# Performance work log

Hardware: AMD Instinct MI355X
Metric: run time of the kernel (lower is better)

Reference implementation:

```python
import jax, jax.numpy as jnp
import numpy as np

DIM = 1024
HIDDEN = 4096
NUM_EXPERTS = 8
TOP_K = 2
T = 8192


def setup_inputs() -> dict:
    key = jax.random.key(0)
    ks = jax.random.split(key, 5)
    scale = 0.02
    x = jax.random.normal(ks[0], (T, DIM), dtype=jnp.float32)
    gate_w = jax.random.normal(ks[1], (NUM_EXPERTS, DIM), dtype=jnp.float32) * scale  # Linear weight [out,in]
    w1 = jax.random.normal(ks[2], (NUM_EXPERTS, HIDDEN, DIM), dtype=jnp.float32) * scale
    w2 = jax.random.normal(ks[3], (NUM_EXPERTS, DIM, HIDDEN), dtype=jnp.float32) * scale
    w3 = jax.random.normal(ks[4], (NUM_EXPERTS, HIDDEN, DIM), dtype=jnp.float32) * scale
    return {"x": x, "gate_w": gate_w, "w1": w1, "w2": w2, "w3": w3}


def reference(x, gate_w, w1, w2, w3):
    # Router: softmax over all experts, take top-2, renormalize.
    logits = jnp.einsum('td,ed->te', x, gate_w)            # [T, E]
    probs = jax.nn.softmax(logits, axis=-1)
    topw, topi = jax.lax.top_k(probs, TOP_K)               # [T, 2]
    topw = topw / jnp.sum(topw, axis=-1, keepdims=True)
    out = jnp.zeros_like(x)
    num_experts = w1.shape[0]
    for e in range(num_experts):
        # combine weight for expert e per token (0 if not routed here)
        w_e = jnp.sum(jnp.where(topi == e, topw, 0.0), axis=-1)   # [T]
        h = jax.nn.silu(x @ w1[e].T) * (x @ w3[e].T)              # [T, HIDDEN]
        out = out + w_e[:, None] * (h @ w2[e].T)                  # [T, DIM]
    return out
```

## Files before the change

### kernel.cpp

```cpp
#include <hip/hip_runtime.h>
#include <hip/hip_bf16.h>
#include <cstdint>
#include <cstddef>

#define TK 8192
#define DIM 1024
#define HID 4096
#define NE 8

typedef __attribute__((ext_vector_type(8))) __bf16 bfrag;
typedef __attribute__((ext_vector_type(4))) float ffrag;

static __device__ __forceinline__ ushort f2bf(float f) {
    union { float f; uint32_t u; } v; v.f = f;
    uint32_t r = (v.u + 0x7fffu + ((v.u >> 16) & 1u)) >> 16;
    return (ushort)r;
}

static __device__ __forceinline__ uint4 pack8(float4 a, float4 b) {
    union { ushort u[8]; uint4 q; } pk;
    pk.u[0] = f2bf(a.x); pk.u[1] = f2bf(a.y); pk.u[2] = f2bf(a.z); pk.u[3] = f2bf(a.w);
    pk.u[4] = f2bf(b.x); pk.u[5] = f2bf(b.y); pk.u[6] = f2bf(b.z); pk.u[7] = f2bf(b.w);
    return pk.q;
}

static __device__ __forceinline__ void gld16(const ushort* g, ushort* l) {
    __builtin_amdgcn_global_load_lds(
        (const __attribute__((address_space(1))) unsigned int*)g,
        (__attribute__((address_space(3))) unsigned int*)l, 16, 0, 0);
}

#define BARRIER() asm volatile("s_barrier" ::: "memory")
#define WAITVM(N) asm volatile("s_waitcnt vmcnt(" #N ")" ::: "memory")

#define LDSIDX(r, kc) ((((r) >> 3) << 8) + ((kc) << 6) + (((r) & 7) << 3))
#define SLOT_R(s)  ((((s) >> 5) << 3) | ((s) & 7))
#define SLOT_KC(s) (((s) >> 3) & 3)

__global__ __launch_bounds__(256) void k_cvt(const float* __restrict__ src,
                                             ushort* __restrict__ dst, int n8) {
    int i = blockIdx.x * blockDim.x + threadIdx.x;
    if (i >= n8) return;
    const float4* p = (const float4*)src + (size_t)i * 2;
    ((uint4*)dst)[i] = pack8(p[0], p[1]);
}

__global__ __launch_bounds__(256) void k_router(const float* __restrict__ x,
                                                const float* __restrict__ gw,
                                                int* __restrict__ topi, float* __restrict__ topw) {
    int t = blockIdx.x * 4 + (threadIdx.x >> 6);
    int lane = threadIdx.x & 63;
    if (t >= TK) return;
    double acc[NE];
#pragma unroll
    for (int e = 0; e < NE; ++e) acc[e] = 0.0;
    const float* xr = x + (size_t)t * DIM;
    for (int k = lane; k < DIM; k += 64) {
        double xv = (double)xr[k];
#pragma unroll
        for (int e = 0; e < NE; ++e) acc[e] += xv * (double)gw[e * DIM + k];
    }
#pragma unroll
    for (int e = 0; e < NE; ++e) {
#pragma unroll
        for (int off = 32; off > 0; off >>= 1) acc[e] += __shfl_xor(acc[e], off);
    }
    if (lane == 0) {
        int i1 = 0;
#pragma unroll
        for (int e = 1; e < NE; ++e) if (acc[e] > acc[i1]) i1 = e;
        int i2 = (i1 == 0) ? 1 : 0;
#pragma unroll
        for (int e = 0; e < NE; ++e) if (e != i1 && acc[e] > acc[i2]) i2 = e;
        double w = 1.0 / (1.0 + exp(acc[i2] - acc[i1]));
        topi[t * 2 + 0] = i1; topi[t * 2 + 1] = i2;
        topw[t * 2 + 0] = (float)w; topw[t * 2 + 1] = (float)(1.0 - w);
    }
}

__global__ void k_count(const int* __restrict__ topi, int* __restrict__ counts) {
    int i = blockIdx.x * blockDim.x + threadIdx.x;
    if (i < 2 * TK) atomicAdd(&counts[topi[i]], 1);
}

__global__ void k_scan(const int* __restrict__ counts, int* __restrict__ offs,
                       int* __restrict__ cursor,
                       int* __restrict__ desc256, int* __restrict__ nd256,
                       int* __restrict__ desc128, int* __restrict__ nd128) {
    if (threadIdx.x == 0 && blockIdx.x == 0) {
        int s = 0, dA = 0, dB = 0;
        for (int e = 0; e < NE; ++e) {
            offs[e] = s; cursor[e] = s;
            int tA = (counts[e] + 255) >> 8;
            for (int t = 0; t < tA; ++t) desc256[dA++] = (e << 16) | t;
            int tB = (counts[e] + 127) >> 7;
            for (int t = 0; t < tB; ++t) desc128[dB++] = (e << 16) | t;
            s += counts[e];
        }
        offs[NE] = s;
        nd256[0] = dA; nd128[0] = dB;
    }
}

__global__ void k_scatter(const int* __restrict__ topi, const float* __restrict__ topw,
                          int* __restrict__ cursor, int* __restrict__ perm, float* __restrict__ pw) {
    int t = blockIdx.x * blockDim.x + threadIdx.x;
    if (t >= TK) return;
#pragma unroll
    for (int k = 0; k < 2; ++k) {
        int e = topi[t * 2 + k];
        int pos = atomicAdd(&cursor[e], 1);
        perm[pos] = t; pw[pos] = topw[t * 2 + k];
    }
}

__global__ __launch_bounds__(512, 2) void k_ffn1(const ushort* __restrict__ xb,
                                                 const ushort* __restrict__ w1b,
                                                 const ushort* __restrict__ w3b,
                                                 const int* __restrict__ offs,
                                                 const int* __restrict__ perm,
                                                 const int* __restrict__ desc,
                                                 const int* __restrict__ nd_g,
                                                 ushort* __restrict__ H) {
    __shared__ ushort lA[2 * 16384];
    __shared__ ushort lB[2 * 16384];
    __shared__ int lTok[256];

    const int tid = threadIdx.x;
    const int lane = tid & 63, wid = tid >> 6;
    const int l15 = lane & 15, kcc = lane >> 4;
    const int mw = wid >> 2;
    const int wn = (wid & 3) * 64;
    const int mwoff = mw * 8192;
    const int wid512 = wid * 512;

    const int NT1 = DIM / 64;
    const int nitems = nd_g[0] << 5;

    int aoff[4], boff[4];
#pragma unroll
    for (int i = 0; i < 4; ++i) aoff[i] = LDSIDX(i * 16 + l15, kcc);
#pragma unroll
    for (int j = 0; j < 4; ++j) {
        int brow = wn + j * 16 + l15;
        boff[j] = ((brow >> 7) << 13) + LDSIDX(brow & 127, kcc);
    }

    const int rS = SLOT_R(tid & 511), kcS = SLOT_KC(tid & 511);

    bfrag a[4], br[4][2];
    ffrag acc[8][4];

#pragma unroll 1
    for (int w = blockIdx.x; w < nitems; w += (int)gridDim.x) {
        __syncthreads();
        const int de = desc[w >> 5];
        const int e = de >> 16, mt = de & 0xffff, nt = w & 31;
        const int m0 = offs[e] + (mt << 8);
        const int nrows = min(256, offs[e + 1] - m0);
        if (tid < 256) lTok[tid] = (tid < nrows) ? perm[m0 + tid] : perm[m0];
        __syncthreads();

        const ushort* pA_[2]; const ushort* pB_[2];
        {
            const size_t ebase = (size_t)e * HID * DIM;
#pragma unroll
            for (int h = 0; h < 2; ++h) {
                pA_[h] = xb + (size_t)lTok[h * 128 + rS] * DIM + kcS * 8;
                int brow = h * 128 + rS;
                int gg = brow >> 4;
                int hc = nt * 128 + (((gg >> 1) << 4) | (brow & 15));
                pB_[h] = ((gg & 1) ? w3b : w1b) + ebase + (size_t)hc * DIM + kcS * 8;
            }
        }

#pragma unroll
        for (int i = 0; i < 8; ++i)
#pragma unroll
            for (int j = 0; j < 4; ++j) acc[i][j] = (ffrag)0.f;

#define SGA1(DB, HH, TT) do { if ((TT) < NT1) { \
            gld16(pA_[HH] + (TT) * 64,      lA + (DB) * 16384 + (HH) * 8192 + wid512); \
            gld16(pA_[HH] + (TT) * 64 + 32, lA + (DB) * 16384 + (HH) * 8192 + 4096 + wid512); } } while (0)
#define SGB1(DB, HH, TT) do { if ((TT) < NT1) { \
            gld16(pB_[HH] + (TT) * 64,      lB + (DB) * 16384 + (HH) * 8192 + wid512); \
            gld16(pB_[HH] + (TT) * 64 + 32, lB + (DB) * 16384 + (HH) * 8192 + 4096 + wid512); } } while (0)
#define RDB1(DB) do { _Pragma("unroll") for (int j = 0; j < 4; ++j) { \
            br[j][0] = *(const bfrag*)&lB[(DB) * 16384 + boff[j]]; \
            br[j][1] = *(const bfrag*)&lB[(DB) * 16384 + boff[j] + 4096]; } } while (0)
#define RDA1(DB, Q, S) do { _Pragma("unroll") for (int i = 0; i < 4; ++i) \
            a[i] = *(const bfrag*)&lA[(DB) * 16384 + mwoff + (S) * 4096 + (Q) * 2048 + aoff[i]]; } while (0)
#define MM1(Q, S) do { __builtin_amdgcn_s_setprio(1); \
            _Pragma("unroll") for (int i = 0; i < 4; ++i) \
            _Pragma("unroll") for (int j = 0; j < 4; ++j) \
                acc[(Q) * 4 + i][j] = __builtin_amdgcn_mfma_f32_16x16x32_bf16(a[i], br[j][S], acc[(Q) * 4 + i][j], 0, 0, 0); \
            __builtin_amdgcn_s_setprio(0); } while (0)
#define PH1(DB, Q, S, BL, STG, WT) do { \
            if (BL) RDB1(DB); RDA1(DB, Q, S); STG; WT; BARRIER(); MM1(Q, S); BARRIER(); } while (0)

        SGA1(0, 0, 0); SGA1(0, 1, 0); SGB1(0, 0, 0); SGB1(0, 1, 0);
        SGB1(1, 0, 1); SGB1(1, 1, 1);
        WAITVM(4);
        BARRIER();

#pragma unroll 1
        for (int it = 0; it < NT1 / 2; ++it) {
            const int t1 = 2 * it + 1, t2 = 2 * it + 2, t3 = 2 * it + 3;
            const bool last = (it == NT1 / 2 - 1);
            PH1(0, 0, 0, 1, SGA1(1, 0, t1), );
            PH1(0, 1, 0, 0, SGA1(1, 1, t1), );
            PH1(0, 0, 1, 0, SGB1(0, 0, t2), );
            PH1(0, 1, 1, 0, SGB1(0, 1, t2), if (last) { WAITVM(0); } else { WAITVM(4); });
            PH1(1, 0, 0, 1, SGA1(0, 0, t2), );
            PH1(1, 1, 0, 0, SGA1(0, 1, t2), );
            PH1(1, 0, 1, 0, SGB1(1, 0, t3), );
            PH1(1, 1, 1, 0, SGB1(1, 1, t3), if (last) { WAITVM(0); } else { WAITVM(4); });
        }
#undef PH1
#undef MM1
#undef RDA1
#undef RDB1
#undef SGB1
#undef SGA1

#pragma unroll
        for (int i = 0; i < 8; ++i) {
            int rbase = mw * 128 + i * 16 + ((lane >> 4) << 2);
#pragma unroll
            for (int q = 0; q < 4; ++q) {
                int rl = rbase + q;
                if (rl >= nrows) continue;
                size_t rowoff = (size_t)(m0 + rl) * HID;
#pragma unroll
                for (int jf = 0; jf < 4; jf += 2) {
                    int gg = (wn >> 4) + jf;
                    int col = nt * 128 + ((gg >> 1) << 4) + l15;
                    float h1 = acc[i][jf][q], h3 = acc[i][jf + 1][q];
                    H[rowoff + col] = f2bf((h1 / (1.f + __expf(-h1))) * h3);
                }
            }
        }
    }
}

__global__ __launch_bounds__(512, 2) void k_ffn2(const ushort* __restrict__ Hs,
                                                 const ushort* __restrict__ w2b,
                                                 const int* __restrict__ offs,
                                                 const int* __restrict__ perm,
                                                 const float* __restrict__ pw,
                                                 const int* __restrict__ desc,
                                                 const int* __restrict__ nd_g,
                                                 float* __restrict__ out) {
    __shared__ ushort lA[2 * 8192];
    __shared__ ushort lB[2 * 16384];
    __shared__ int lTok[128];
    __shared__ float lPw[128];

    const int tid = threadIdx.x;
    const int lane = tid & 63, wid = tid >> 6;
    const int l15 = lane & 15, kcc = lane >> 4;
    const int mw = wid >> 2;
    const int wn = (wid & 3) * 64;
    const int wid512 = wid * 512;

    const int NT2 = HID / 64;
    const int nitems = nd_g[0] << 2;

    int aoff[4], boff[4];
#pragma unroll
    for (int i = 0; i < 4; ++i) aoff[i] = LDSIDX(mw * 64 + i * 16 + l15, kcc);
#pragma unroll
    for (int j = 0; j < 4; ++j) {
        int brow = wn + j * 16 + l15;
        boff[j] = ((brow >> 7) << 13) + LDSIDX(brow & 127, kcc);
    }

    const int rS = SLOT_R(tid & 511), kcS = SLOT_KC(tid & 511);

    bfrag a[4], br[4][2];
    ffrag acc[4][4];

#pragma unroll 1
    for (int w = blockIdx.x; w < nitems; w += (int)gridDim.x) {
        __syncthreads();
        const int de = desc[w >> 2];
        const int e = de >> 16, mt = de & 0xffff, nt = w & 3;
        const int m0 = offs[e] + (mt << 7);
        const int nrows = min(128, offs[e + 1] - m0);
        if (tid < 128) {
            bool v = tid < nrows;
            lTok[tid] = v ? perm[m0 + tid] : 0;
            lPw[tid]  = v ? pw[m0 + tid] : 0.f;
        }
        __syncthreads();

        int posA = m0 + rS; if (posA > 2 * TK - 1) posA = 2 * TK - 1;
        const ushort* pA_ = Hs + (size_t)posA * HID + kcS * 8;
        const ushort* pB_[2];
        {
            const size_t ebase = (size_t)e * DIM * HID;
#pragma unroll
            for (int h = 0; h < 2; ++h)
                pB_[h] = w2b + ebase + (size_t)(nt * 256 + h * 128 + rS) * HID + kcS * 8;
        }

#pragma unroll
        for (int i = 0; i < 4; ++i)
#pragma unroll
            for (int j = 0; j < 4; ++j) acc[i][j] = (ffrag)0.f;

#define SGA2(DB, SUB, TT) do { if ((TT) < NT2) \
            gld16(pA_ + (TT) * 64 + (SUB) * 32, lA + (DB) * 8192 + (SUB) * 4096 + wid512); } while (0)
#define SGB2(DB, HH, SUB, TT) do { if ((TT) < NT2) \
            gld16(pB_[HH] + (TT) * 64 + (SUB) * 32, lB + (DB) * 16384 + (HH) * 8192 + (SUB) * 4096 + wid512); } while (0)
#define RDB2(DB) do { _Pragma("unroll") for (int j = 0; j < 4; ++j) { \
            br[j][0] = *(const bfrag*)&lB[(DB) * 16384 + boff[j]]; \
            br[j][1] = *(const bfrag*)&lB[(DB) * 16384 + boff[j] + 4096]; } } while (0)
#define RDA2(DB, S) do { _Pragma("unroll") for (int i = 0; i < 4; ++i) \
            a[i] = *(const bfrag*)&lA[(DB) * 8192 + (S) * 4096 + aoff[i]]; } while (0)
#define MM2(S) do { __builtin_amdgcn_s_setprio(1); \
            _Pragma("unroll") for (int i = 0; i < 4; ++i) \
            _Pragma("unroll") for (int j = 0; j < 4; ++j) \
                acc[i][j] = __builtin_amdgcn_mfma_f32_16x16x32_bf16(a[i], br[j][S], acc[i][j], 0, 0, 0); \
            __builtin_amdgcn_s_setprio(0); } while (0)

        SGA2(0, 0, 0); SGA2(0, 1, 0);
        SGB2(0, 0, 0, 0); SGB2(0, 0, 1, 0); SGB2(0, 1, 0, 0); SGB2(0, 1, 1, 0);
        SGB2(1, 0, 0, 1); SGB2(1, 0, 1, 1); SGB2(1, 1, 0, 1);
        WAITVM(3);
        BARRIER();

#pragma unroll 1
        for (int it = 0; it < NT2 / 2; ++it) {
            const int t1 = 2 * it + 1, t2 = 2 * it + 2, t3 = 2 * it + 3;
            const bool last = (it == NT2 / 2 - 1);
            RDB2(0); RDA2(0, 0);
            SGB2(1, 1, 1, t1); SGA2(1, 0, t1); SGA2(1, 1, t1);
            BARRIER(); MM2(0); BARRIER();
            RDA2(0, 1);
            SGB2(0, 0, 0, t2); SGB2(0, 0, 1, t2); SGB2(0, 1, 0, t2);
            if (last) { WAITVM(0); } else { WAITVM(3); }
            BARRIER(); MM2(1); BARRIER();
            RDB2(1); RDA2(1, 0);
            SGB2(0, 1, 1, t2); SGA2(0, 0, t2); SGA2(0, 1, t2);
            BARRIER(); MM2(0); BARRIER();
            RDA2(1, 1);
            SGB2(1, 0, 0, t3); SGB2(1, 0, 1, t3); SGB2(1, 1, 0, t3);
            if (last) { WAITVM(0); } else { WAITVM(3); }
            BARRIER(); MM2(1); BARRIER();
        }
#undef MM2
#undef RDA2
#undef RDB2
#undef SGB2
#undef SGA2

#pragma unroll
        for (int i = 0; i < 4; ++i) {
            int rbase = mw * 64 + i * 16 + ((lane >> 4) << 2);
#pragma unroll
            for (int q = 0; q < 4; ++q) {
                int rl = rbase + q;
                if (rl >= nrows) continue;
                int tok = lTok[rl];
                float wgt = lPw[rl];
                size_t rowoff = (size_t)tok * DIM;
#pragma unroll
                for (int j = 0; j < 4; ++j) {
                    int col = nt * 256 + wn + j * 16 + l15;
                    atomicAdd(&out[rowoff + col], acc[i][j][q] * wgt);
                }
            }
        }
    }
}

extern "C" void kernel_launch(void* const* d_in, const int* in_sizes, int n_in,
                              void* d_out, int out_size, void* d_ws, size_t ws_size,
                              hipStream_t stream) {
    const float* x  = (const float*)d_in[0];
    const float* gw = (const float*)d_in[1];
    const float* w1 = (const float*)d_in[2];
    const float* w2 = (const float*)d_in[3];
    const float* w3 = (const float*)d_in[4];
    float* out = (float*)d_out;

    char* ws = (char*)d_ws;
    int*    topi    = (int*)(ws + 0);
    float*  topw    = (float*)(ws + 65536);
    int*    perm    = (int*)(ws + 131072);
    float*  pw      = (float*)(ws + 196608);
    int*    counts  = (int*)(ws + 262144);
    int*    offs    = (int*)(ws + 262144 + 256);
    int*    cursor  = (int*)(ws + 262144 + 512);
    int*    nd256   = (int*)(ws + 262144 + 768);
    int*    nd128   = (int*)(ws + 262144 + 772);
    int*    desc256 = (int*)(ws + 262144 + 1024);
    int*    desc128 = (int*)(ws + 262144 + 2048);

    const size_t OFF_XB = 524288;
    const size_t OFF_H  = OFF_XB + 16777216;
    const size_t OFF_WA = OFF_H + 134217728;
    const size_t OFF_WB = OFF_WA + 67108864;

    ushort* xb  = (ushort*)(ws + OFF_XB);
    ushort* H   = (ushort*)(ws + OFF_H);
    ushort* wA  = (ushort*)(ws + OFF_WA);
    ushort* wB  = (ushort*)(ws + OFF_WB);

    hipMemsetAsync(counts, 0, 32, stream);
    hipMemsetAsync(out, 0, (size_t)out_size * sizeof(float), stream);

    k_router<<<dim3(TK / 4), 256, 0, stream>>>(x, gw, topi, topw);
    k_count<<<dim3((2 * TK) / 256), 256, 0, stream>>>(topi, counts);
    k_scan<<<dim3(1), 64, 0, stream>>>(counts, offs, cursor, desc256, nd256, desc128, nd128);
    k_scatter<<<dim3(TK / 256), 256, 0, stream>>>(topi, topw, cursor, perm, pw);

    k_cvt<<<dim3((TK * DIM / 8) / 256), 256, 0, stream>>>(x, xb, TK * DIM / 8);
    k_cvt<<<dim3((NE * HID * DIM / 8) / 256), 256, 0, stream>>>(w1, wA, NE * HID * DIM / 8);
    k_cvt<<<dim3((NE * HID * DIM / 8) / 256), 256, 0, stream>>>(w3, wB, NE * HID * DIM / 8);

    k_ffn1<<<dim3(256), 512, 0, stream>>>(xb, wA, wB, offs, perm, desc256, nd256, H);

    k_cvt<<<dim3((NE * DIM * HID / 8) / 256), 256, 0, stream>>>(w2, wA, NE * DIM * HID / 8);

    k_ffn2<<<dim3(512), 512, 0, stream>>>(H, wA, offs, perm, pw, desc128, nd128, out);
}
```

Baseline: 1.029 ms.

## Switch MoE GEMMs to one-tile-per-block grids with triple-buffered FFN2 pipeline

Replaces the persistent grid-stride loops in both expert GEMM kernels with one work tile per block and early exit for unused descriptors, so the hardware scheduler balances tiles. FFN2 moves to a three-stage LDS pipeline with one block per CU. The router now counts expert assignments itself, dropping the count kernel, and the x/w1/w3 conversions are merged into one launch. The cost is more launched blocks that exit immediately, and lower FFN2 occupancy in exchange for deeper prefetch.

```diff
diff --git a/kernel.cpp b/kernel.cpp
--- a/kernel.cpp
+++ b/kernel.cpp
@@ -45,9 +45,25 @@
     ((uint4*)dst)[i] = pack8(p[0], p[1]);
 }
 
+__global__ __launch_bounds__(256) void k_cvt3(const float* __restrict__ x,
+                                              const float* __restrict__ w1,
+                                              const float* __restrict__ w3,
+                                              ushort* __restrict__ xb,
+                                              ushort* __restrict__ wA,
+                                              ushort* __restrict__ wB) {
+    int i = blockIdx.x * blockDim.x + threadIdx.x;
+    const float* src; ushort* dst; int j;
+    if (i < (1 << 20))                  { src = x;  dst = xb; j = i; }
+    else if (i < (1 << 20) + (1 << 22)) { src = w1; dst = wA; j = i - (1 << 20); }
+    else                                { src = w3; dst = wB; j = i - (1 << 20) - (1 << 22); }
+    const float4* p = (const float4*)src + (size_t)j * 2;
+    ((uint4*)dst)[j] = pack8(p[0], p[1]);
+}
+
 __global__ __launch_bounds__(256) void k_router(const float* __restrict__ x,
                                                 const float* __restrict__ gw,
-                                                int* __restrict__ topi, float* __restrict__ topw) {
+                                                int* __restrict__ topi, float* __restrict__ topw,
+                                                int* __restrict__ counts) {
     int t = blockIdx.x * 4 + (threadIdx.x >> 6);
     int lane = threadIdx.x & 63;
     if (t >= TK) return;
@@ -75,12 +91,9 @@
         double w = 1.0 / (1.0 + exp(acc[i2] - acc[i1]));
         topi[t * 2 + 0] = i1; topi[t * 2 + 1] = i2;
         topw[t * 2 + 0] = (float)w; topw[t * 2 + 1] = (float)(1.0 - w);
-    }
-}
-
-__global__ void k_count(const int* __restrict__ topi, int* __restrict__ counts) {
-    int i = blockIdx.x * blockDim.x + threadIdx.x;
-    if (i < 2 * TK) atomicAdd(&counts[topi[i]], 1);
+        atomicAdd(&counts[i1], 1);
+        atomicAdd(&counts[i2], 1);
+    }
 }
 
 __global__ void k_scan(const int* __restrict__ counts, int* __restrict__ offs,
@@ -103,7 +116,8 @@
 }
 
 __global__ void k_scatter(const int* __restrict__ topi, const float* __restrict__ topw,
-                          int* __restrict__ cursor, int* __restrict__ perm, float* __restrict__ pw) {
+                          int* __restrict__ cursor, int* __restrict__ perm,
+                          float* __restrict__ pw) {
     int t = blockIdx.x * blockDim.x + threadIdx.x;
     if (t >= TK) return;
 #pragma unroll
@@ -122,6 +136,11 @@
                                                  const int* __restrict__ desc,
                                                  const int* __restrict__ nd_g,
                                                  ushort* __restrict__ H) {
+    const int b = blockIdx.x;
+    const int d = ((b >> 8) << 3) | (b & 7);
+    const int nt = (b >> 3) & 31;
+    if (d >= nd_g[0]) return;
+
     __shared__ ushort lA[2 * 16384];
     __shared__ ushort lB[2 * 16384];
     __shared__ int lTok[256];
@@ -135,7 +154,6 @@
     const int wid512 = wid * 512;
 
     const int NT1 = DIM / 64;
-    const int nitems = nd_g[0] << 5;
 
     int aoff[4], boff[4];
 #pragma unroll
@@ -151,71 +169,68 @@
     bfrag a[4], br[4][2];
     ffrag acc[8][4];
 
+    const int de = desc[d];
+    const int e = de >> 16, mt = de & 0xffff;
+    const int m0 = offs[e] + (mt << 8);
+    const int nrows = min(256, offs[e + 1] - m0);
+    if (tid < 256) lTok[tid] = (tid < nrows) ? perm[m0 + tid] : perm[m0];
+    __syncthreads();
+
+    const ushort* pA_[2]; const ushort* pB_[2];
+    {
+        const size_t ebase = (size_t)e * HID * DIM;
+#pragma unroll
+        for (int h = 0; h < 2; ++h) {
+            pA_[h] = xb + (size_t)lTok[h * 128 + rS] * DIM + kcS * 8;
+            int brow = h * 128 + rS;
+            int gg = brow >> 4;
+            int hc = nt * 128 + (((gg >> 1) << 4) | (brow & 15));
+            pB_[h] = ((gg & 1) ? w3b : w1b) + ebase + (size_t)hc * DIM + kcS * 8;
+        }
+    }
+
+#pragma unroll
+    for (int i = 0; i < 8; ++i)
+#pragma unroll
+        for (int j = 0; j < 4; ++j) acc[i][j] = (ffrag)0.f;
+
+#define SGA1(DB, HH, TT) do { if ((TT) < NT1) { \
+        gld16(pA_[HH] + (TT) * 64,      lA + (DB) * 16384 + (HH) * 8192 + wid512); \
+        gld16(pA_[HH] + (TT) * 64 + 32, lA + (DB) * 16384 + (HH) * 8192 + 4096 + wid512); } } while (0)
+#define SGB1(DB, HH, TT) do { if ((TT) < NT1) { \
+        gld16(pB_[HH] + (TT) * 64,      lB + (DB) * 16384 + (HH) * 8192 + wid512); \
+        gld16(pB_[HH] + (TT) * 64 + 32, lB + (DB) * 16384 + (HH) * 8192 + 4096 + wid512); } } while (0)
+#define RDB1(DB) do { _Pragma("unroll") for (int j = 0; j < 4; ++j) { \
+        br[j][0] = *(const bfrag*)&lB[(DB) * 16384 + boff[j]]; \
+        br[j][1] = *(const bfrag*)&lB[(DB) * 16384 + boff[j] + 4096]; } } while (0)
+#define RDA1(DB, Q, S) do { _Pragma("unroll") for (int i = 0; i < 4; ++i) \
+        a[i] = *(const bfrag*)&lA[(DB) * 16384 + mwoff + (S) * 4096 + (Q) * 2048 + aoff[i]]; } while (0)
+#define MM1(Q, S) do { __builtin_amdgcn_s_setprio(1); \
+        _Pragma("unroll") for (int i = 0; i < 4; ++i) \
+        _Pragma("unroll") for (int j = 0; j < 4; ++j) \
+            acc[(Q) * 4 + i][j] = __builtin_amdgcn_mfma_f32_16x16x32_bf16(a[i], br[j][S], acc[(Q) * 4 + i][j], 0, 0, 0); \
+        __builtin_amdgcn_s_setprio(0); } while (0)
+#define PH1(DB, Q, S, BL, STG, WT) do { \
+        if (BL) RDB1(DB); RDA1(DB, Q, S); STG; WT; BARRIER(); MM1(Q, S); BARRIER(); } while (0)
+
+    SGA1(0, 0, 0); SGA1(0, 1, 0); SGB1(0, 0, 0); SGB1(0, 1, 0);
+    SGB1(1, 0, 1); SGB1(1, 1, 1);
+    WAITVM(4);
+    BARRIER();
+
 #pragma unroll 1
-    for (int w = blockIdx.x; w < nitems; w += (int)gridDim.x) {
-        __syncthreads();
-        const int de = desc[w >> 5];
-        const int e = de >> 16, mt = de & 0xffff, nt = w & 31;
-        const int m0 = offs[e] + (mt << 8);
-        const int nrows = min(256, offs[e + 1] - m0);
-        if (tid < 256) lTok[tid] = (tid < nrows) ? perm[m0 + tid] : perm[m0];
-        __syncthreads();
-
-        const ushort* pA_[2]; const ushort* pB_[2];
-        {
-            const size_t ebase = (size_t)e * HID * DIM;
-#pragma unroll
-            for (int h = 0; h < 2; ++h) {
-                pA_[h] = xb + (size_t)lTok[h * 128 + rS] * DIM + kcS * 8;
-                int brow = h * 128 + rS;
-                int gg = brow >> 4;
-                int hc = nt * 128 + (((gg >> 1) << 4) | (brow & 15));
-                pB_[h] = ((gg & 1) ? w3b : w1b) + ebase + (size_t)hc * DIM + kcS * 8;
-            }
-        }
-
-#pragma unroll
-        for (int i = 0; i < 8; ++i)
-#pragma unroll
-            for (int j = 0; j < 4; ++j) acc[i][j] = (ffrag)0.f;
-
-#define SGA1(DB, HH, TT) do { if ((TT) < NT1) { \
-            gld16(pA_[HH] + (TT) * 64,      lA + (DB) * 16384 + (HH) * 8192 + wid512); \
-            gld16(pA_[HH] + (TT) * 64 + 32, lA + (DB) * 16384 + (HH) * 8192 + 4096 + wid512); } } while (0)
-#define SGB1(DB, HH, TT) do { if ((TT) < NT1) { \
-            gld16(pB_[HH] + (TT) * 64,      lB + (DB) * 16384 + (HH) * 8192 + wid512); \
-            gld16(pB_[HH] + (TT) * 64 + 32, lB + (DB) * 16384 + (HH) * 8192 + 4096 + wid512); } } while (0)
-#define RDB1(DB) do { _Pragma("unroll") for (int j = 0; j < 4; ++j) { \
-            br[j][0] = *(const bfrag*)&lB[(DB) * 16384 + boff[j]]; \
-            br[j][1] = *(const bfrag*)&lB[(DB) * 16384 + boff[j] + 4096]; } } while (0)
-#define RDA1(DB, Q, S) do { _Pragma("unroll") for (int i = 0; i < 4; ++i) \
-            a[i] = *(const bfrag*)&lA[(DB) * 16384 + mwoff + (S) * 4096 + (Q) * 2048 + aoff[i]]; } while (0)
-#define MM1(Q, S) do { __builtin_amdgcn_s_setprio(1); \
-            _Pragma("unroll") for (int i = 0; i < 4; ++i) \
-            _Pragma("unroll") for (int j = 0; j < 4; ++j) \
-                acc[(Q) * 4 + i][j] = __builtin_amdgcn_mfma_f32_16x16x32_bf16(a[i], br[j][S], acc[(Q) * 4 + i][j], 0, 0, 0); \
-            __builtin_amdgcn_s_setprio(0); } while (0)
-#define PH1(DB, Q, S, BL, STG, WT) do { \
-            if (BL) RDB1(DB); RDA1(DB, Q, S); STG; WT; BARRIER(); MM1(Q, S); BARRIER(); } while (0)
-
-        SGA1(0, 0, 0); SGA1(0, 1, 0); SGB1(0, 0, 0); SGB1(0, 1, 0);
-        SGB1(1, 0, 1); SGB1(1, 1, 1);
-        WAITVM(4);
-        BARRIER();
-
-#pragma unroll 1
-        for (int it = 0; it < NT1 / 2; ++it) {
-            const int t1 = 2 * it + 1, t2 = 2 * it + 2, t3 = 2 * it + 3;
-            const bool last = (it == NT1 / 2 - 1);
-            PH1(0, 0, 0, 1, SGA1(1, 0, t1), );
-            PH1(0, 1, 0, 0, SGA1(1, 1, t1), );
-            PH1(0, 0, 1, 0, SGB1(0, 0, t2), );
-            PH1(0, 1, 1, 0, SGB1(0, 1, t2), if (last) { WAITVM(0); } else { WAITVM(4); });
-            PH1(1, 0, 0, 1, SGA1(0, 0, t2), );
-            PH1(1, 1, 0, 0, SGA1(0, 1, t2), );
-            PH1(1, 0, 1, 0, SGB1(1, 0, t3), );
-            PH1(1, 1, 1, 0, SGB1(1, 1, t3), if (last) { WAITVM(0); } else { WAITVM(4); });
-        }
+    for (int it = 0; it < NT1 / 2; ++it) {
+        const int t1 = 2 * it + 1, t2 = 2 * it + 2, t3 = 2 * it + 3;
+        const bool last = (it == NT1 / 2 - 1);
+        PH1(0, 0, 0, 1, SGA1(1, 0, t1), );
+        PH1(0, 1, 0, 0, SGA1(1, 1, t1), );
+        PH1(0, 0, 1, 0, SGB1(0, 0, t2), );
+        PH1(0, 1, 1, 0, SGB1(0, 1, t2), if (last) { WAITVM(0); } else { WAITVM(4); });
+        PH1(1, 0, 0, 1, SGA1(0, 0, t2), );
+        PH1(1, 1, 0, 0, SGA1(0, 1, t2), );
+        PH1(1, 0, 1, 0, SGB1(1, 0, t3), );
+        PH1(1, 1, 1, 0, SGB1(1, 1, t3), if (last) { WAITVM(0); } else { WAITVM(4); });
+    }
 #undef PH1
 #undef MM1
 #undef RDA1
@@ -224,26 +239,25 @@
 #undef SGA1
 
 #pragma unroll
-        for (int i = 0; i < 8; ++i) {
-            int rbase = mw * 128 + i * 16 + ((lane >> 4) << 2);
-#pragma unroll
-            for (int q = 0; q < 4; ++q) {
-                int rl = rbase + q;
-                if (rl >= nrows) continue;
-                size_t rowoff = (size_t)(m0 + rl) * HID;
-#pragma unroll
-                for (int jf = 0; jf < 4; jf += 2) {
-                    int gg = (wn >> 4) + jf;
-                    int col = nt * 128 + ((gg >> 1) << 4) + l15;
-                    float h1 = acc[i][jf][q], h3 = acc[i][jf + 1][q];
-                    H[rowoff + col] = f2bf((h1 / (1.f + __expf(-h1))) * h3);
-                }
+    for (int i = 0; i < 8; ++i) {
+        int rbase = mw * 128 + i * 16 + ((lane >> 4) << 2);
+#pragma unroll
+        for (int q = 0; q < 4; ++q) {
+            int rl = rbase + q;
+            if (rl >= nrows) continue;
+            size_t rowoff = (size_t)(m0 + rl) * HID;
+#pragma unroll
+            for (int jf = 0; jf < 4; jf += 2) {
+                int gg = (wn >> 4) + jf;
+                int col = nt * 128 + ((gg >> 1) << 4) + l15;
+                float h1 = acc[i][jf][q], h3 = acc[i][jf + 1][q];
+                H[rowoff + col] = f2bf((h1 / (1.f + __expf(-h1))) * h3);
             }
         }
     }
 }
 
-__global__ __launch_bounds__(512, 2) void k_ffn2(const ushort* __restrict__ Hs,
+__global__ __launch_bounds__(512, 1) void k_ffn2(const ushort* __restrict__ Hs,
                                                  const ushort* __restrict__ w2b,
                                                  const int* __restrict__ offs,
                                                  const int* __restrict__ perm,
@@ -251,8 +265,12 @@
                                                  const int* __restrict__ desc,
                                                  const int* __restrict__ nd_g,
                                                  float* __restrict__ out) {
-    __shared__ ushort lA[2 * 8192];
-    __shared__ ushort lB[2 * 16384];
+    const int b = blockIdx.x;
+    const int d = b >> 2, nt = b & 3;
+    if (d >= nd_g[0]) return;
+
+    __shared__ ushort lA[3 * 8192];
+    __shared__ ushort lB[3 * 16384];
     __shared__ int lTok[128];
     __shared__ float lPw[128];
 
@@ -264,7 +282,6 @@
     const int wid512 = wid * 512;
 
     const int NT2 = HID / 64;
-    const int nitems = nd_g[0] << 2;
 
     int aoff[4], boff[4];
 #pragma unroll
@@ -280,75 +297,68 @@
     bfrag a[4], br[4][2];
     ffrag acc[4][4];
 
+    const int de = desc[d];
+    const int e = de >> 16, mt = de & 0xffff;
+    const int m0 = offs[e] + (mt << 7);
+    const int nrows = min(128, offs[e + 1] - m0);
+    if (tid < 128) {
+        bool v = tid < nrows;
+        lTok[tid] = v ? perm[m0 + tid] : 0;
+        lPw[tid]  = v ? pw[m0 + tid] : 0.f;
+    }
+    __syncthreads();
+
+    int posA = m0 + rS; if (posA > 2 * TK - 1) posA = 2 * TK - 1;
+    const ushort* pA_ = Hs + (size_t)posA * HID + kcS * 8;
+    const ushort* pB_[2];
+    {
+        const size_t ebase = (size_t)e * DIM * HID;
+#pragma unroll
+        for (int h = 0; h < 2; ++h)
+            pB_[h] = w2b + ebase + (size_t)(nt * 256 + h * 128 + rS) * HID + kcS * 8;
+    }
+
+#pragma unroll
+    for (int i = 0; i < 4; ++i)
+#pragma unroll
+        for (int j = 0; j < 4; ++j) acc[i][j] = (ffrag)0.f;
+
+#define SGA2(BUF, S, TT) do { if ((TT) < NT2) \
+        gld16(pA_ + (TT) * 64 + (S) * 32, lA + (BUF) * 8192 + (S) * 4096 + wid512); } while (0)
+#define SGB2(BUF, HH, S, TT) do { if ((TT) < NT2) \
+        gld16(pB_[HH] + (TT) * 64 + (S) * 32, lB + (BUF) * 16384 + (HH) * 8192 + (S) * 4096 + wid512); } while (0)
+#define RDB2(BUF) do { _Pragma("unroll") for (int j = 0; j < 4; ++j) { \
+        br[j][0] = *(const bfrag*)&lB[(BUF) * 16384 + boff[j]]; \
+        br[j][1] = *(const bfrag*)&lB[(BUF) * 16384 + boff[j] + 4096]; } } while (0)
+#define RDA2(BUF, S) do { _Pragma("unroll") for (int i = 0; i < 4; ++i) \
+        a[i] = *(const bfrag*)&lA[(BUF) * 8192 + (S) * 4096 + aoff[i]]; } while (0)
+#define MM2(S) do { __builtin_amdgcn_s_setprio(1); \
+        _Pragma("unroll") for (int i = 0; i < 4; ++i) \
+        _Pragma("unroll") for (int j = 0; j < 4; ++j) \
+            acc[i][j] = __builtin_amdgcn_mfma_f32_16x16x32_bf16(a[i], br[j][S], acc[i][j], 0, 0, 0); \
+        __builtin_amdgcn_s_setprio(0); } while (0)
+
+    SGA2(0, 0, 0); SGA2(0, 1, 0);
+    SGB2(0, 0, 0, 0); SGB2(0, 0, 1, 0); SGB2(0, 1, 0, 0); SGB2(0, 1, 1, 0);
+    SGA2(1, 0, 1); SGA2(1, 1, 1);
+    SGB2(1, 0, 0, 1); SGB2(1, 0, 1, 1); SGB2(1, 1, 0, 1); SGB2(1, 1, 1, 1);
+    WAITVM(6);
+    BARRIER();
+
+    int cur = 0, nx2 = 2;
 #pragma unroll 1
-    for (int w = blockIdx.x; w < nitems; w += (int)gridDim.x) {
-        __syncthreads();
-        const int de = desc[w >> 2];
-        const int e = de >> 16, mt = de & 0xffff, nt = w & 3;
-        const int m0 = offs[e] + (mt << 7);
-        const int nrows = min(128, offs[e + 1] - m0);
-        if (tid < 128) {
-            bool v = tid < nrows;
-            lTok[tid] = v ? perm[m0 + tid] : 0;
-            lPw[tid]  = v ? pw[m0 + tid] : 0.f;
-        }
-        __syncthreads();
-
-        int posA = m0 + rS; if (posA > 2 * TK - 1) posA = 2 * TK - 1;
-        const ushort* pA_ = Hs + (size_t)posA * HID + kcS * 8;
-        const ushort* pB_[2];
-        {
-            const size_t ebase = (size_t)e * DIM * HID;
-#pragma unroll
-            for (int h = 0; h < 2; ++h)
-                pB_[h] = w2b + ebase + (size_t)(nt * 256 + h * 128 + rS) * HID + kcS * 8;
-        }
-
-#pragma unroll
-        for (int i = 0; i < 4; ++i)
-#pragma unroll
-            for (int j = 0; j < 4; ++j) acc[i][j] = (ffrag)0.f;
-
-#define SGA2(DB, SUB, TT) do { if ((TT) < NT2) \
-            gld16(pA_ + (TT) * 64 + (SUB) * 32, lA + (DB) * 8192 + (SUB) * 4096 + wid512); } while (0)
-#define SGB2(DB, HH, SUB, TT) do { if ((TT) < NT2) \
-            gld16(pB_[HH] + (TT) * 64 + (SUB) * 32, lB + (DB) * 16384 + (HH) * 8192 + (SUB) * 4096 + wid512); } while (0)
-#define RDB2(DB) do { _Pragma("unroll") for (int j = 0; j < 4; ++j) { \
-            br[j][0] = *(const bfrag*)&lB[(DB) * 16384 + boff[j]]; \
-            br[j][1] = *(const bfrag*)&lB[(DB) * 16384 + boff[j] + 4096]; } } while (0)
-#define RDA2(DB, S) do { _Pragma("unroll") for (int i = 0; i < 4; ++i) \
-            a[i] = *(const bfrag*)&lA[(DB) * 8192 + (S) * 4096 + aoff[i]]; } while (0)
-#define MM2(S) do { __builtin_amdgcn_s_setprio(1); \
-            _Pragma("unroll") for (int i = 0; i < 4; ++i) \
-            _Pragma("unroll") for (int j = 0; j < 4; ++j) \
-                acc[i][j] = __builtin_amdgcn_mfma_f32_16x16x32_bf16(a[i], br[j][S], acc[i][j], 0, 0, 0); \
-            __builtin_amdgcn_s_setprio(0); } while (0)
-
-        SGA2(0, 0, 0); SGA2(0, 1, 0);
-        SGB2(0, 0, 0, 0); SGB2(0, 0, 1, 0); SGB2(0, 1, 0, 0); SGB2(0, 1, 1, 0);
-        SGB2(1, 0, 0, 1); SGB2(1, 0, 1, 1); SGB2(1, 1, 0, 1);
-        WAITVM(3);
-        BARRIER();
-
-#pragma unroll 1
-        for (int it = 0; it < NT2 / 2; ++it) {
-            const int t1 = 2 * it + 1, t2 = 2 * it + 2, t3 = 2 * it + 3;
-            const bool last = (it == NT2 / 2 - 1);
-            RDB2(0); RDA2(0, 0);
-            SGB2(1, 1, 1, t1); SGA2(1, 0, t1); SGA2(1, 1, t1);
-            BARRIER(); MM2(0); BARRIER();
-            RDA2(0, 1);
-            SGB2(0, 0, 0, t2); SGB2(0, 0, 1, t2); SGB2(0, 1, 0, t2);
-            if (last) { WAITVM(0); } else { WAITVM(3); }
-            BARRIER(); MM2(1); BARRIER();
-            RDB2(1); RDA2(1, 0);
-            SGB2(0, 1, 1, t2); SGA2(0, 0, t2); SGA2(0, 1, t2);
-            BARRIER(); MM2(0); BARRIER();
-            RDA2(1, 1);
-            SGB2(1, 0, 0, t3); SGB2(1, 0, 1, t3); SGB2(1, 1, 0, t3);
-            if (last) { WAITVM(0); } else { WAITVM(3); }
-            BARRIER(); MM2(1); BARRIER();
-        }
+    for (int t = 0; t < NT2; ++t) {
+        const int tt = t + 2;
+        RDB2(cur); RDA2(cur, 0);
+        SGA2(nx2, 0, tt); SGA2(nx2, 1, tt); SGB2(nx2, 0, 0, tt);
+        BARRIER(); MM2(0); BARRIER();
+        RDA2(cur, 1);
+        SGB2(nx2, 0, 1, tt); SGB2(nx2, 1, 0, tt); SGB2(nx2, 1, 1, tt);
+        if (tt < NT2) { WAITVM(6); } else { WAITVM(0); }
+        BARRIER(); MM2(1); BARRIER();
+        cur = (cur == 2) ? 0 : cur + 1;
+        nx2 = (nx2 == 2) ? 0 : nx2 + 1;
+    }
 #undef MM2
 #undef RDA2
 #undef RDB2
@@ -356,20 +366,19 @@
 #undef SGA2
 
 #pragma unroll
-        for (int i = 0; i < 4; ++i) {
-            int rbase = mw * 64 + i * 16 + ((lane >> 4) << 2);
-#pragma unroll
-            for (int q = 0; q < 4; ++q) {
-                int rl = rbase + q;
-                if (rl >= nrows) continue;
-                int tok = lTok[rl];
-                float wgt = lPw[rl];
-                size_t rowoff = (size_t)tok * DIM;
-#pragma unroll
-                for (int j = 0; j < 4; ++j) {
-                    int col = nt * 256 + wn + j * 16 + l15;
-                    atomicAdd(&out[rowoff + col], acc[i][j][q] * wgt);
-                }
+    for (int i = 0; i < 4; ++i) {
+        int rbase = mw * 64 + i * 16 + ((lane >> 4) << 2);
+#pragma unroll
+        for (int q = 0; q < 4; ++q) {
+            int rl = rbase + q;
+            if (rl >= nrows) continue;
+            int tok = lTok[rl];
+            float wgt = lPw[rl];
+            size_t rowoff = (size_t)tok * DIM;
+#pragma unroll
+            for (int j = 0; j < 4; ++j) {
+                int col = nt * 256 + wn + j * 16 + l15;
+                atomicAdd(&out[rowoff + col], acc[i][j][q] * wgt);
             }
         }
     }
@@ -398,7 +407,7 @@
     int*    desc256 = (int*)(ws + 262144 + 1024);
     int*    desc128 = (int*)(ws + 262144 + 2048);
 
-    const size_t OFF_XB = 524288;
+    const size_t OFF_XB = 655360;
     const size_t OFF_H  = OFF_XB + 16777216;
     const size_t OFF_WA = OFF_H + 134217728;
     const size_t OFF_WB = OFF_WA + 67108864;
@@ -411,18 +420,15 @@
     hipMemsetAsync(counts, 0, 32, stream);
     hipMemsetAsync(out, 0, (size_t)out_size * sizeof(float), stream);
 
-    k_router<<<dim3(TK / 4), 256, 0, stream>>>(x, gw, topi, topw);
-    k_count<<<dim3((2 * TK) / 256), 256, 0, stream>>>(topi, counts);
+    k_router<<<dim3(TK / 4), 256, 0, stream>>>(x, gw, topi, topw, counts);
     k_scan<<<dim3(1), 64, 0, stream>>>(counts, offs, cursor, desc256, nd256, desc128, nd128);
     k_scatter<<<dim3(TK / 256), 256, 0, stream>>>(topi, topw, cursor, perm, pw);
 
-    k_cvt<<<dim3((TK * DIM / 8) / 256), 256, 0, stream>>>(x, xb, TK * DIM / 8);
-    k_cvt<<<dim3((NE * HID * DIM / 8) / 256), 256, 0, stream>>>(w1, wA, NE * HID * DIM / 8);
-    k_cvt<<<dim3((NE * HID * DIM / 8) / 256), 256, 0, stream>>>(w3, wB, NE * HID * DIM / 8);
-
-    k_ffn1<<<dim3(256), 512, 0, stream>>>(xb, wA, wB, offs, perm, desc256, nd256, H);
+    k_cvt3<<<dim3(36864), 256, 0, stream>>>(x, w1, w3, xb, wA, wB);
+
+    k_ffn1<<<dim3(9 * 256), 512, 0, stream>>>(xb, wA, wB, offs, perm, desc256, nd256, H);
 
     k_cvt<<<dim3((NE * DIM * HID / 8) / 256), 256, 0, stream>>>(w2, wA, NE * DIM * HID / 8);
 
-    k_ffn2<<<dim3(512), 512, 0, stream>>>(H, wA, offs, perm, pw, desc128, nd128, out);
-}
+    k_ffn2<<<dim3(136 * 4), 512, 0, stream>>>(H, wA, offs, perm, pw, desc128, nd128, out);
+}
```

New measurement: 1.128 ms. 9.6% more time.
